# Kernel tuning notes

Measured on AMD Instinct MI355X. Metric: run time of the kernel, lower is better.

The kernel has to match this reference:

```python
import jax, jax.numpy as jnp
import numpy as np

EPS = 1e-5

def _relu6(x):
    return jnp.clip(x, 0.0, 6.0)

def _bn(x, g, b, m, v):
    # inference-mode batchnorm folded into scale/shift
    inv = g / jnp.sqrt(v + EPS)
    return x * inv[None, :, None, None] + (b - m * inv)[None, :, None, None]

def _patch_pw(x, W):
    # per-patch 1x1 conv. x: [B,Ci,H,Wd], W: [B,Fh,Fw,Co,Ci]
    B, C, H, Wd = x.shape
    Fh, Fw = W.shape[1:3]
    ph, pw = H // Fh, Wd // Fw
    xb = x.reshape(B, C, Fh, ph, Fw, pw)
    yb = jnp.einsum('bfgoc,bcfpgq->bofpgq', W, xb)
    return yb.reshape(B, W.shape[3], H, Wd)

def _patch_dw3(x, K):
    # per-patch depthwise 3x3, reflect pad applied to the full map (halo from neighbors).
    # x: [B,C,H,Wd], K: [B,Fh,Fw,C,3,3]
    B, C, H, Wd = x.shape
    Fh, Fw = K.shape[1:3]
    ph, pw = H // Fh, Wd // Fw
    xp = jnp.pad(x, ((0, 0), (0, 0), (1, 1), (1, 1)), mode='reflect')
    acc = jnp.zeros((B, C, Fh, ph, Fw, pw), x.dtype)
    for dy in range(3):
        for dx in range(3):
            xs = xp[:, :, dy:dy + H, dx:dx + Wd].reshape(B, C, Fh, ph, Fw, pw)
            k = K[:, :, :, :, dy, dx].transpose(0, 3, 1, 2)  # [B,C,Fh,Fw]
            acc = acc + xs * k[:, :, :, None, :, None]
    return acc.reshape(B, C, H, Wd)

def setup_inputs() -> dict:
    key = jax.random.key(0)
    ks = jax.random.split(key, 16)
    B, Cin, H, Wd = 4, 64, 128, 128
    hidden, Cout, Fh, Fw = 384, 64, 16, 16
    n_params = hidden * Cin + hidden * 9 + Cout * hidden  # 52608
    return {
        'x': jax.random.normal(ks[0], (B, Cin, H, Wd), jnp.float32),
        'w': jax.random.normal(ks[1], (B, n_params, Fh, Fw), jnp.float32) * 0.05,
        'g1': jax.random.uniform(ks[2], (hidden,), jnp.float32),
        'b1': jax.random.normal(ks[3], (hidden,), jnp.float32),
        'm1': jax.random.normal(ks[4], (hidden,), jnp.float32),
        'v1': jax.random.uniform(ks[5], (hidden,), jnp.float32),
        'g2': jax.random.uniform(ks[6], (hidden,), jnp.float32),
        'b2': jax.random.normal(ks[7], (hidden,), jnp.float32),
        'm2': jax.random.normal(ks[8], (hidden,), jnp.float32),
        'v2': jax.random.uniform(ks[9], (hidden,), jnp.float32),
        'g3': jax.random.uniform(ks[10], (Cout,), jnp.float32),
        'b3': jax.random.normal(ks[11], (Cout,), jnp.float32),
        'm3': jax.random.normal(ks[12], (Cout,), jnp.float32),
        'v3': jax.random.uniform(ks[13], (Cout,), jnp.float32),
    }

def reference(x, w, g1, b1, m1, v1, g2, b2, m2, v2, g3, b3, m3, v3):
    B, Cin = x.shape[:2]
    Fh, Fw = w.shape[2:]
    hidden = g1.shape[0]
    Cout = g3.shape[0]
    n1 = hidden * Cin
    n2 = hidden * 9
    wg = w.transpose(0, 2, 3, 1)  # [B,Fh,Fw,P]
    W1 = wg[..., :n1].reshape(B, Fh, Fw, hidden, Cin)
    K2 = wg[..., n1:n1 + n2].reshape(B, Fh, Fw, hidden, 3, 3)
    W3 = wg[..., n1 + n2:].reshape(B, Fh, Fw, Cout, hidden)
    h = _relu6(_bn(_patch_pw(x, W1), g1, b1, m1, v1))
    h = _relu6(_bn(_patch_dw3(h, K2), g2, b2, m2, v2))
    h = _bn(_patch_pw(h, W3), g3, b3, m3, v3)
    return x + h  # use_res_connect: stride==1 and in_nc==out_nc
```

## Files before the change

### kernel.cpp

```cpp
#include <hip/hip_runtime.h>

#define EPSV 1e-5f

constexpr int CIN = 64, NH = 128, NW = 128, HID = 384, COUT = 64;
constexpr int N1 = HID * CIN;
constexpr int N2 = HID * 9;
constexpr int NP = N1 + N2 + COUT * HID;

using bf16x8 = __attribute__((ext_vector_type(8))) short;
using f32x4  = __attribute__((ext_vector_type(4))) float;

__device__ __forceinline__ unsigned short f2bf(float f) {
  unsigned int u = __float_as_uint(f);
  u = (u + 0x7fffu + ((u >> 16) & 1u)) >> 16;
  return (unsigned short)u;
}
__device__ __forceinline__ unsigned int pack2(float a, float b) {
  return (unsigned int)f2bf(a) | ((unsigned int)f2bf(b) << 16);
}
__device__ __forceinline__ float ulo(unsigned int u) { return __uint_as_float(u << 16); }
__device__ __forceinline__ float uhi(unsigned int u) { return __uint_as_float(u & 0xffff0000u); }
__device__ __forceinline__ float clamp6(float v) { return fminf(fmaxf(v, 0.f), 6.f); }

__global__ __launch_bounds__(256) void k0_transpose(
    const float* __restrict__ x, unsigned short* __restrict__ xT) {
  __shared__ unsigned short xls[64][66];
  const int t = threadIdx.x;
  const int xh = blockIdx.x, y = blockIdx.y, b = blockIdx.z;
#pragma unroll
  for (int it = 0; it < 4; ++it) {
    int i = it * 256 + t;
    int xq = i & 15, c = i >> 4;
    float4 v = *reinterpret_cast<const float4*>(
        &x[((size_t)(b * CIN + c) * NH + y) * NW + xh * 64 + xq * 4]);
    *(unsigned int*)&xls[c][xq * 4]     = pack2(v.x, v.y);
    *(unsigned int*)&xls[c][xq * 4 + 2] = pack2(v.z, v.w);
  }
  __syncthreads();
#pragma unroll
  for (int it = 0; it < 4; ++it) {
    int i = it * 256 + t;
    int cq = i & 15, px = i >> 4;
    ushort4 o;
    o.x = xls[cq * 4 + 0][px];
    o.y = xls[cq * 4 + 1][px];
    o.z = xls[cq * 4 + 2][px];
    o.w = xls[cq * 4 + 3][px];
    *reinterpret_cast<ushort4*>(
        &xT[((size_t)(b * NH + y) * NW + xh * 64 + px) * 64 + cq * 4]) = o;
  }
}

__global__ __launch_bounds__(256) void k1_pw1(
    const float* __restrict__ w, const unsigned short* __restrict__ xT,
    const float* __restrict__ g1, const float* __restrict__ b1,
    const float* __restrict__ m1, const float* __restrict__ v1,
    unsigned short* __restrict__ h1T) {
  __shared__ unsigned short Wpk[2048 * 8];

  const unsigned int id = blockIdx.x;
  const int fbq = id & 7;
  const unsigned int rest = id >> 3;
  const int hgrp = rest % 24, q = rest / 24;
  const int fb = q * 8 + fbq;
  const int f = fb & 15, b = fb >> 4;
  const int h0 = hgrp * 16;

  const int t = threadIdx.x;
  const int lane = t & 63, wv = t >> 6;
  const int quad = lane >> 4, nn = lane & 15;
  const int pxi = wv * 16 + nn;

#pragma unroll
  for (int it = 0; it < 8; ++it) {
    int i = it * 256 + t;
    int gq = i & 3, cp = (i >> 2) & 31, hid = i >> 7;
    const float* wp =
        &w[((size_t)b * NP + (h0 + hid) * CIN + cp * 2) * 256 + f * 16 + gq * 4];
    float4 A  = *reinterpret_cast<const float4*>(wp);
    float4 Bv = *reinterpret_cast<const float4*>(wp + 256);
    int kc = cp >> 4, qd = (cp >> 2) & 3, j = (cp & 3) * 2;
    int hs = hid ^ (2 * qd) ^ gq;
    const float* Af = (const float*)&A;
    const float* Bf = (const float*)&Bv;
#pragma unroll
    for (int k = 0; k < 4; ++k) {
      int g = gq * 4 + k;
      *(unsigned int*)&Wpk[(((g * 2 + kc) * 4 + qd) * 16 + hs) * 8 + j] =
          pack2(Af[k], Bf[k]);
    }
  }

  float iv1[4], sh1[4];
#pragma unroll
  for (int jj = 0; jj < 4; ++jj) {
    int hid = h0 + quad * 4 + jj;
    float iv = g1[hid] * rsqrtf(v1[hid] + EPSV);
    iv1[jj] = iv;
    sh1[jj] = b1[hid] - m1[hid] * iv;
  }
  __syncthreads();

  const int y = f * 8 + (pxi >> 3);
  const size_t rowbase = ((size_t)b * NH + y) * NW;

  for (int g = 0; g < 16; ++g) {
    const int xc = g * 8 + (pxi & 7);
    const unsigned short* xp = &xT[(rowbase + xc) * 64];
    f32x4 acc = {0.f, 0.f, 0.f, 0.f};
    const int hs = nn ^ (2 * quad) ^ (g >> 2);
#pragma unroll
    for (int kc = 0; kc < 2; ++kc) {
      bf16x8 af = *reinterpret_cast<const bf16x8*>(
          &Wpk[(((g * 2 + kc) * 4 + quad) * 16 + hs) * 8]);
      bf16x8 bfr = *reinterpret_cast<const bf16x8*>(&xp[kc * 32 + quad * 8]);
      acc = __builtin_amdgcn_mfma_f32_16x16x32_bf16(af, bfr, acc, 0, 0, 0);
    }
    ushort4 o;
    o.x = f2bf(clamp6(acc[0] * iv1[0] + sh1[0]));
    o.y = f2bf(clamp6(acc[1] * iv1[1] + sh1[1]));
    o.z = f2bf(clamp6(acc[2] * iv1[2] + sh1[2]));
    o.w = f2bf(clamp6(acc[3] * iv1[3] + sh1[3]));
    *reinterpret_cast<ushort4*>(&h1T[(rowbase + xc) * HID + h0 + quad * 4]) = o;
  }
}

__global__ __launch_bounds__(256) void k2_fused(
    const float* __restrict__ x, const float* __restrict__ w,
    const float* __restrict__ g2, const float* __restrict__ b2v,
    const float* __restrict__ m2, const float* __restrict__ v2,
    const float* __restrict__ g3, const float* __restrict__ b3v,
    const float* __restrict__ m3, const float* __restrict__ v3,
    const unsigned short* __restrict__ h1T, float* __restrict__ out) {
  __shared__ unsigned short tile[10][34][40];
  __shared__ unsigned short h2s[256][40];
  __shared__ unsigned short W3p[512 * 8];
  __shared__ unsigned short k2w[4][9][40];
  __shared__ float iv2s[HID], sh2s[HID];

  const unsigned int id = blockIdx.x;
  const int fbq = id & 7;
  const unsigned int rest = id >> 3;
  const int gang = rest & 7, q = rest >> 3;
  const int fb = q * 8 + fbq;
  const int f = fb & 15, b = fb >> 4;
  const int gq = gang >> 1, ch = gang & 1;
  const int c0 = gq * 32;

  const int t = threadIdx.x;
  const int lane = t & 63, wv = t >> 6;
  const int quad = lane >> 4, nn = lane & 15;

  for (int i = t; i < HID; i += 256) {
    float iv = g2[i] * rsqrtf(v2[i] + EPSV);
    iv2s[i] = iv;
    sh2s[i] = b2v[i] - m2[i] * iv;
  }

  float iv3[2][4], sh3[2][4];
#pragma unroll
  for (int cot = 0; cot < 2; ++cot)
#pragma unroll
    for (int jj = 0; jj < 4; ++jj) {
      int co = ch * 32 + cot * 16 + quad * 4 + jj;
      float iv = g3[co] * rsqrtf(v3[co] + EPSV);
      iv3[cot][jj] = iv;
      sh3[cot][jj] = b3v[co] - m3[co] * iv;
    }

  f32x4 acc[2][4];
#pragma unroll
  for (int cot = 0; cot < 2; ++cot)
#pragma unroll
    for (int nt = 0; nt < 4; ++nt) acc[cot][nt] = (f32x4){0.f, 0.f, 0.f, 0.f};

  const int glt = t >> 6, rt = (t >> 3) & 7, ct = t & 7;

  for (int hc = 0; hc < 12; ++hc) {
    const int hb = hc * 32;
    __syncthreads();

#pragma unroll
    for (int it = 0; it < 6; ++it) {
      int idx = it * 256 + t;
      if (idx < 1360) {
        int qh = idx & 3, pxid = idx >> 2;
        int r = pxid / 34, col = pxid - r * 34;
        int yy = f * 8 - 1 + r;
        yy = (yy < 0) ? -yy : ((yy > 127) ? 254 - yy : yy);
        int xc = c0 - 1 + col;
        xc = (xc < 0) ? 1 : ((xc > 127) ? 126 : xc);
        uint4 v = *reinterpret_cast<const uint4*>(
            &h1T[(((size_t)b * NH + yy) * NW + xc) * HID + hb + qh * 8]);
        *reinterpret_cast<uint4*>(&tile[r][col][qh * 8]) = v;
      }
    }
    for (int i = t; i < 288; i += 256) {
      int hh = i / 9, tap = i - hh * 9;
      const float4 wv4 = *reinterpret_cast<const float4*>(
          &w[((size_t)b * NP + N1 + (hb + hh) * 9 + tap) * 256 + f * 16 +
             gq * 4]);
      k2w[0][tap][hh] = f2bf(wv4.x);
      k2w[1][tap][hh] = f2bf(wv4.y);
      k2w[2][tap][hh] = f2bf(wv4.z);
      k2w[3][tap][hh] = f2bf(wv4.w);
    }
#pragma unroll
    for (int it = 0; it < 2; ++it) {
      int i = it * 256 + t;
      int hhp = i & 15, co = i >> 4;
      const float* wp = &w[((size_t)b * NP + N1 + N2 + (ch * 32 + co) * HID +
                            hb + hhp * 2) * 256 + f * 16 + gq * 4];
      float4 A  = *reinterpret_cast<const float4*>(wp);
      float4 Bv = *reinterpret_cast<const float4*>(wp + 256);
      int qd = (hhp * 2) >> 3, j = (hhp * 2) & 7, cot = co >> 4;
      int cb = co & 15;
      const float* Af = (const float*)&A;
      const float* Bf = (const float*)&Bv;
#pragma unroll
      for (int k = 0; k < 4; ++k) {
        int cop = cb ^ (2 * qd) ^ k;
        *(unsigned int*)&W3p[(((k * 2 + cot) * 4 + qd) * 16 + cop) * 8 + j] =
            pack2(Af[k], Bf[k]);
      }
    }
    __syncthreads();

#pragma unroll
    for (int hg = 0; hg < 4; ++hg) {
      float d[8] = {0.f, 0.f, 0.f, 0.f, 0.f, 0.f, 0.f, 0.f};
#pragma unroll
      for (int dy = 0; dy < 3; ++dy)
#pragma unroll
        for (int dx = 0; dx < 3; ++dx) {
          const uint4 tv = *reinterpret_cast<const uint4*>(
              &tile[rt + dy][glt * 8 + ct + dx][hg * 8]);
          const uint4 kv =
              *reinterpret_cast<const uint4*>(&k2w[glt][dy * 3 + dx][hg * 8]);
          d[0] += ulo(tv.x) * ulo(kv.x); d[1] += uhi(tv.x) * uhi(kv.x);
          d[2] += ulo(tv.y) * ulo(kv.y); d[3] += uhi(tv.y) * uhi(kv.y);
          d[4] += ulo(tv.z) * ulo(kv.z); d[5] += uhi(tv.z) * uhi(kv.z);
          d[6] += ulo(tv.w) * ulo(kv.w); d[7] += uhi(tv.w) * uhi(kv.w);
        }
      uint4 o4;
      unsigned int op[4];
#pragma unroll
      for (int j2 = 0; j2 < 4; ++j2) {
        int ha = hb + hg * 8 + j2 * 2;
        float oa = clamp6(d[j2 * 2] * iv2s[ha] + sh2s[ha]);
        float ob = clamp6(d[j2 * 2 + 1] * iv2s[ha + 1] + sh2s[ha + 1]);
        op[j2] = (unsigned int)f2bf(oa) | ((unsigned int)f2bf(ob) << 16);
      }
      o4.x = op[0]; o4.y = op[1]; o4.z = op[2]; o4.w = op[3];
      *reinterpret_cast<uint4*>(&h2s[t][hg * 8]) = o4;
    }
    __syncthreads();

    {
      const int gl = wv;
      const int cop = nn ^ (2 * quad) ^ gl;
      bf16x8 a0 = *reinterpret_cast<const bf16x8*>(
          &W3p[(((gl * 2 + 0) * 4 + quad) * 16 + cop) * 8]);
      bf16x8 a1 = *reinterpret_cast<const bf16x8*>(
          &W3p[(((gl * 2 + 1) * 4 + quad) * 16 + cop) * 8]);
#pragma unroll
      for (int nt = 0; nt < 4; ++nt) {
        bf16x8 bfr = *reinterpret_cast<const bf16x8*>(
            &h2s[gl * 64 + nt * 16 + nn][quad * 8]);
        acc[0][nt] = __builtin_amdgcn_mfma_f32_16x16x32_bf16(a0, bfr, acc[0][nt], 0, 0, 0);
        acc[1][nt] = __builtin_amdgcn_mfma_f32_16x16x32_bf16(a1, bfr, acc[1][nt], 0, 0, 0);
      }
    }
  }

#pragma unroll
  for (int cot = 0; cot < 2; ++cot)
#pragma unroll
    for (int nt = 0; nt < 4; ++nt) {
      int pxl = nt * 16 + nn;
      int y = f * 8 + (pxl >> 3);
      int xc = c0 + wv * 8 + (pxl & 7);
#pragma unroll
      for (int jj = 0; jj < 4; ++jj) {
        int co = ch * 32 + cot * 16 + quad * 4 + jj;
        size_t adr = ((size_t)(b * COUT + co) * NH + y) * NW + xc;
        out[adr] = acc[cot][nt][jj] * iv3[cot][jj] + sh3[cot][jj] + x[adr];
      }
    }
}

extern "C" void kernel_launch(void* const* d_in, const int* in_sizes, int n_in,
                              void* d_out, int out_size, void* d_ws,
                              size_t ws_size, hipStream_t stream) {
  (void)in_sizes; (void)n_in; (void)out_size; (void)ws_size;
  const float* x  = (const float*)d_in[0];
  const float* w  = (const float*)d_in[1];
  const float* g1 = (const float*)d_in[2];
  const float* b1 = (const float*)d_in[3];
  const float* m1 = (const float*)d_in[4];
  const float* v1 = (const float*)d_in[5];
  const float* g2 = (const float*)d_in[6];
  const float* b2 = (const float*)d_in[7];
  const float* m2 = (const float*)d_in[8];
  const float* v2 = (const float*)d_in[9];
  const float* g3 = (const float*)d_in[10];
  const float* b3 = (const float*)d_in[11];
  const float* m3 = (const float*)d_in[12];
  const float* v3 = (const float*)d_in[13];
  float* out = (float*)d_out;
  unsigned short* h1T = (unsigned short*)d_ws;
  unsigned short* xT = (unsigned short*)d_out;

  k0_transpose<<<dim3(2, 128, 4), 256, 0, stream>>>(x, xT);
  k1_pw1<<<dim3(1536), 256, 0, stream>>>(w, xT, g1, b1, m1, v1, h1T);
  k2_fused<<<dim3(512), 256, 0, stream>>>(x, w, g2, b2, m2, v2, g3, b3, m3, v3,
                                          h1T, out);
}
```

Baseline: 460.3 us.

## Register-prefetch next hidden chunk's tile and weights to overlap global loads with compute

Moves the global loads for the next 32-channel hidden chunk (h1 halo tile, depthwise kernels, W3 slice) into registers issued right after the LDS-store barrier, so they overlap with the depthwise and MFMA work of the current chunk. Address computations are hoisted out of the loop into precomputed pointers that advance each iteration. __syncthreads is replaced by an explicit lgkmcnt wait plus s_barrier, which does not wait on outstanding global loads. This costs many extra VGPRs for the prefetch buffers and pointers, which may reduce occupancy.

```diff
diff --git a/kernel.cpp b/kernel.cpp
--- a/kernel.cpp
+++ b/kernel.cpp
@@ -21,6 +21,12 @@
 __device__ __forceinline__ float ulo(unsigned int u) { return __uint_as_float(u << 16); }
 __device__ __forceinline__ float uhi(unsigned int u) { return __uint_as_float(u & 0xffff0000u); }
 __device__ __forceinline__ float clamp6(float v) { return fminf(fmaxf(v, 0.f), 6.f); }
+
+#define BAR_LDS()                                             \
+  do {                                                        \
+    asm volatile("s_waitcnt lgkmcnt(0)" ::: "memory");        \
+    __builtin_amdgcn_s_barrier();                             \
+  } while (0)
 
 __global__ __launch_bounds__(256) void k0_transpose(
     const float* __restrict__ x, unsigned short* __restrict__ xT) {
@@ -176,55 +182,97 @@
 
   const int glt = t >> 6, rt = (t >> 3) & 7, ct = t & 7;
 
+  const unsigned short* tsrc[6];
+  unsigned short* tdst[6];
+  bool tac[6];
+#pragma unroll
+  for (int it = 0; it < 6; ++it) {
+    int idx = it * 256 + t;
+    tac[it] = (idx < 1360);
+    int idc = tac[it] ? idx : 0;
+    int qh = idc & 3, pxid = idc >> 2;
+    int r = pxid / 34, col = pxid - r * 34;
+    int yy = f * 8 - 1 + r;
+    yy = (yy < 0) ? -yy : ((yy > 127) ? 254 - yy : yy);
+    int xc = c0 - 1 + col;
+    xc = (xc < 0) ? 1 : ((xc > 127) ? 126 : xc);
+    tsrc[it] = &h1T[(((size_t)b * NH + yy) * NW + xc) * HID + qh * 8];
+    tdst[it] = &tile[r][col][qh * 8];
+  }
+  const int hh1 = t / 9, tap1 = t - hh1 * 9;
+  const float* ksrc1 = &w[((size_t)b * NP + N1 + t) * 256 + f * 16 + gq * 4];
+  const bool kac2 = (t < 32);
+  const int i2k = 256 + t;
+  const int hh2 = i2k / 9, tap2 = i2k - hh2 * 9;
+  const float* ksrc2 = &w[((size_t)b * NP + N1 + i2k) * 256 + f * 16 + gq * 4];
+  const float* wsrc[2];
+  unsigned int* wdst[2][4];
+#pragma unroll
+  for (int it = 0; it < 2; ++it) {
+    int i = it * 256 + t;
+    int hhp = i & 15, co = i >> 4;
+    wsrc[it] = &w[((size_t)b * NP + N1 + N2 + (ch * 32 + co) * HID + hhp * 2) *
+                      256 + f * 16 + gq * 4];
+    int qd = (hhp * 2) >> 3, j = (hhp * 2) & 7, cot = co >> 4, cb = co & 15;
+#pragma unroll
+    for (int k = 0; k < 4; ++k) {
+      int cop = cb ^ (2 * qd) ^ k;
+      wdst[it][k] =
+          (unsigned int*)&W3p[(((k * 2 + cot) * 4 + qd) * 16 + cop) * 8 + j];
+    }
+  }
+
+  uint4 trg[6];
+  float4 krg1, krg2;
+  float4 wAr[2], wBr[2];
+
+#define PREFETCH()                                                           \
+  do {                                                                       \
+    _Pragma("unroll") for (int pit = 0; pit < 6; ++pit) {                    \
+      if (tac[pit]) trg[pit] = *reinterpret_cast<const uint4*>(tsrc[pit]);   \
+      tsrc[pit] += 32;                                       \
+    }                                                                        \
+    krg1 = *reinterpret_cast<const float4*>(ksrc1);                          \
+    ksrc1 += 73728;                                            \
+    if (kac2) krg2 = *reinterpret_cast<const float4*>(ksrc2);                \
+    ksrc2 += 73728;                                                          \
+    _Pragma("unroll") for (int pit = 0; pit < 2; ++pit) {                    \
+      wAr[pit] = *reinterpret_cast<const float4*>(wsrc[pit]);                \
+      wBr[pit] = *reinterpret_cast<const float4*>(wsrc[pit] + 256);          \
+      wsrc[pit] += 8192;                                         \
+    }                                                                        \
+  } while (0)
+
+  PREFETCH();
+
   for (int hc = 0; hc < 12; ++hc) {
     const int hb = hc * 32;
-    __syncthreads();
-
-#pragma unroll
-    for (int it = 0; it < 6; ++it) {
-      int idx = it * 256 + t;
-      if (idx < 1360) {
-        int qh = idx & 3, pxid = idx >> 2;
-        int r = pxid / 34, col = pxid - r * 34;
-        int yy = f * 8 - 1 + r;
-        yy = (yy < 0) ? -yy : ((yy > 127) ? 254 - yy : yy);
-        int xc = c0 - 1 + col;
-        xc = (xc < 0) ? 1 : ((xc > 127) ? 126 : xc);
-        uint4 v = *reinterpret_cast<const uint4*>(
-            &h1T[(((size_t)b * NH + yy) * NW + xc) * HID + hb + qh * 8]);
-        *reinterpret_cast<uint4*>(&tile[r][col][qh * 8]) = v;
-      }
-    }
-    for (int i = t; i < 288; i += 256) {
-      int hh = i / 9, tap = i - hh * 9;
-      const float4 wv4 = *reinterpret_cast<const float4*>(
-          &w[((size_t)b * NP + N1 + (hb + hh) * 9 + tap) * 256 + f * 16 +
-             gq * 4]);
-      k2w[0][tap][hh] = f2bf(wv4.x);
-      k2w[1][tap][hh] = f2bf(wv4.y);
-      k2w[2][tap][hh] = f2bf(wv4.z);
-      k2w[3][tap][hh] = f2bf(wv4.w);
+    BAR_LDS();
+
+#pragma unroll
+    for (int it = 0; it < 6; ++it)
+      if (tac[it]) *reinterpret_cast<uint4*>(tdst[it]) = trg[it];
+    k2w[0][tap1][hh1] = f2bf(krg1.x);
+    k2w[1][tap1][hh1] = f2bf(krg1.y);
+    k2w[2][tap1][hh1] = f2bf(krg1.z);
+    k2w[3][tap1][hh1] = f2bf(krg1.w);
+    if (kac2) {
+      k2w[0][tap2][hh2] = f2bf(krg2.x);
+      k2w[1][tap2][hh2] = f2bf(krg2.y);
+      k2w[2][tap2][hh2] = f2bf(krg2.z);
+      k2w[3][tap2][hh2] = f2bf(krg2.w);
     }
 #pragma unroll
     for (int it = 0; it < 2; ++it) {
-      int i = it * 256 + t;
-      int hhp = i & 15, co = i >> 4;
-      const float* wp = &w[((size_t)b * NP + N1 + N2 + (ch * 32 + co) * HID +
-                            hb + hhp * 2) * 256 + f * 16 + gq * 4];
-      float4 A  = *reinterpret_cast<const float4*>(wp);
-      float4 Bv = *reinterpret_cast<const float4*>(wp + 256);
-      int qd = (hhp * 2) >> 3, j = (hhp * 2) & 7, cot = co >> 4;
-      int cb = co & 15;
-      const float* Af = (const float*)&A;
-      const float* Bf = (const float*)&Bv;
-#pragma unroll
-      for (int k = 0; k < 4; ++k) {
-        int cop = cb ^ (2 * qd) ^ k;
-        *(unsigned int*)&W3p[(((k * 2 + cot) * 4 + qd) * 16 + cop) * 8 + j] =
-            pack2(Af[k], Bf[k]);
-      }
-    }
-    __syncthreads();
+      const float* Af = (const float*)&wAr[it];
+      const float* Bf = (const float*)&wBr[it];
+#pragma unroll
+      for (int k = 0; k < 4; ++k) *wdst[it][k] = pack2(Af[k], Bf[k]);
+    }
+
+    BAR_LDS();
+
+    if (hc < 11) PREFETCH();
 
 #pragma unroll
     for (int hg = 0; hg < 4; ++hg) {
@@ -254,7 +302,8 @@
       o4.x = op[0]; o4.y = op[1]; o4.z = op[2]; o4.w = op[3];
       *reinterpret_cast<uint4*>(&h2s[t][hg * 8]) = o4;
     }
-    __syncthreads();
+
+    BAR_LDS();
 
     {
       const int gl = wv;
```

After: 492.0 us. 1.07x slower.

## Register-prefetch next chunk's h1 tile and weights to overlap global loads with compute

Applied to the files above, without the earlier changes.

The fused depthwise+pointwise kernel now issues global loads for the next hidden-channel chunk (h1 tile, depthwise taps, W3 weights) into registers right after the LDS stores. Those loads overlap with the depthwise and MFMA compute of the current chunk. Per-thread source and destination addresses are precomputed once and advanced by strides, and __syncthreads is replaced with a waitcnt on LDS only plus a raw barrier. Launch bounds request two blocks per SM, which adds register pressure from the prefetch registers and risks spills.

```diff
diff --git a/kernel.cpp b/kernel.cpp
--- a/kernel.cpp
+++ b/kernel.cpp
@@ -21,6 +21,12 @@
 __device__ __forceinline__ float ulo(unsigned int u) { return __uint_as_float(u << 16); }
 __device__ __forceinline__ float uhi(unsigned int u) { return __uint_as_float(u & 0xffff0000u); }
 __device__ __forceinline__ float clamp6(float v) { return fminf(fmaxf(v, 0.f), 6.f); }
+
+#define BAR_LDS()                                             \
+  do {                                                        \
+    asm volatile("s_waitcnt lgkmcnt(0)" ::: "memory");        \
+    __builtin_amdgcn_s_barrier();                             \
+  } while (0)
 
 __global__ __launch_bounds__(256) void k0_transpose(
     const float* __restrict__ x, unsigned short* __restrict__ xT) {
@@ -125,7 +131,7 @@
   }
 }
 
-__global__ __launch_bounds__(256) void k2_fused(
+__global__ __launch_bounds__(256, 2) void k2_fused(
     const float* __restrict__ x, const float* __restrict__ w,
     const float* __restrict__ g2, const float* __restrict__ b2v,
     const float* __restrict__ m2, const float* __restrict__ v2,
@@ -176,55 +182,121 @@
 
   const int glt = t >> 6, rt = (t >> 3) & 7, ct = t & 7;
 
+#define TGEOM(IDX, SRC, DST)                                          \
+  {                                                                   \
+    int qh = (IDX) & 3, pxid = (IDX) >> 2;                            \
+    int r = pxid / 34, col = pxid - r * 34;                           \
+    int yy = f * 8 - 1 + r;                                           \
+    yy = (yy < 0) ? -yy : ((yy > 127) ? 254 - yy : yy);               \
+    int xc = c0 - 1 + col;                                            \
+    xc = (xc < 0) ? 1 : ((xc > 127) ? 126 : xc);                      \
+    SRC = &h1T[(((size_t)b * NH + yy) * NW + xc) * HID + qh * 8];     \
+    DST = &tile[r][col][qh * 8];                                      \
+  }
+  const unsigned short *ts0, *ts1, *ts2, *ts3, *ts4, *ts5;
+  unsigned short *td0, *td1, *td2, *td3, *td4, *td5;
+  const bool tac5 = (t < 80);
+  TGEOM(t, ts0, td0);
+  TGEOM(256 + t, ts1, td1);
+  TGEOM(512 + t, ts2, td2);
+  TGEOM(768 + t, ts3, td3);
+  TGEOM(1024 + t, ts4, td4);
+  {
+    int idx5 = tac5 ? (1280 + t) : 1359;
+    TGEOM(idx5, ts5, td5);
+  }
+#undef TGEOM
+
+  const int hh1 = t / 9, tap1 = t - hh1 * 9;
+  const float* ksrc1 = &w[((size_t)b * NP + N1 + t) * 256 + f * 16 + gq * 4];
+  const bool kac2 = (t < 32);
+  const int i2k = 256 + t;
+  const int hh2 = i2k / 9, tap2 = i2k - hh2 * 9;
+  const float* ksrc2 = &w[((size_t)b * NP + N1 + i2k) * 256 + f * 16 + gq * 4];
+
+  const float *wsrc0, *wsrc1;
+  unsigned int *wd00, *wd01, *wd02, *wd03, *wd10, *wd11, *wd12, *wd13;
+#define W3GEOM(IT, SRC, D0, D1, D2, D3)                                   \
+  {                                                                      \
+    int i = (IT) * 256 + t;                                              \
+    int hhp = i & 15, co = i >> 4;                                       \
+    SRC = &w[((size_t)b * NP + N1 + N2 + (ch * 32 + co) * HID + hhp * 2) * \
+                 256 + f * 16 + gq * 4];                                 \
+    int qd = (hhp * 2) >> 3, j = (hhp * 2) & 7, cot = co >> 4,           \
+        cb = co & 15;                                                    \
+    D0 = (unsigned int*)&W3p[(((0 * 2 + cot) * 4 + qd) * 16 +            \
+                              (cb ^ (2 * qd) ^ 0)) * 8 + j];             \
+    D1 = (unsigned int*)&W3p[(((1 * 2 + cot) * 4 + qd) * 16 +            \
+                              (cb ^ (2 * qd) ^ 1)) * 8 + j];             \
+    D2 = (unsigned int*)&W3p[(((2 * 2 + cot) * 4 + qd) * 16 +            \
+                              (cb ^ (2 * qd) ^ 2)) * 8 + j];             \
+    D3 = (unsigned int*)&W3p[(((3 * 2 + cot) * 4 + qd) * 16 +            \
+                              (cb ^ (2 * qd) ^ 3)) * 8 + j];             \
+  }
+  W3GEOM(0, wsrc0, wd00, wd01, wd02, wd03);
+  W3GEOM(1, wsrc1, wd10, wd11, wd12, wd13);
+#undef W3GEOM
+
+  uint4 tr0, tr1, tr2, tr3, tr4, tr5;
+  float4 kr1, kr2;
+  float4 wA0, wB0, wA1, wB1;
+
+#define PREFETCH()                                                  \
+  do {                                                              \
+    tr0 = *reinterpret_cast<const uint4*>(ts0); ts0 += 32;          \
+    tr1 = *reinterpret_cast<const uint4*>(ts1); ts1 += 32;          \
+    tr2 = *reinterpret_cast<const uint4*>(ts2); ts2 += 32;          \
+    tr3 = *reinterpret_cast<const uint4*>(ts3); ts3 += 32;          \
+    tr4 = *reinterpret_cast<const uint4*>(ts4); ts4 += 32;          \
+    if (tac5) tr5 = *reinterpret_cast<const uint4*>(ts5);           \
+    ts5 += 32;                                                      \
+    kr1 = *reinterpret_cast<const float4*>(ksrc1); ksrc1 += 73728;  \
+    if (kac2) kr2 = *reinterpret_cast<const float4*>(ksrc2);        \
+    ksrc2 += 73728;                                                 \
+    wA0 = *reinterpret_cast<const float4*>(wsrc0);                  \
+    wB0 = *reinterpret_cast<const float4*>(wsrc0 + 256);            \
+    wsrc0 += 8192;                                                  \
+    wA1 = *reinterpret_cast<const float4*>(wsrc1);                  \
+    wB1 = *reinterpret_cast<const float4*>(wsrc1 + 256);            \
+    wsrc1 += 8192;                                                  \
+  } while (0)
+
+  tr5 = (uint4){0u, 0u, 0u, 0u};
+  kr2 = (float4){0.f, 0.f, 0.f, 0.f};
+  PREFETCH();
+
   for (int hc = 0; hc < 12; ++hc) {
     const int hb = hc * 32;
-    __syncthreads();
-
-#pragma unroll
-    for (int it = 0; it < 6; ++it) {
-      int idx = it * 256 + t;
-      if (idx < 1360) {
-        int qh = idx & 3, pxid = idx >> 2;
-        int r = pxid / 34, col = pxid - r * 34;
-        int yy = f * 8 - 1 + r;
-        yy = (yy < 0) ? -yy : ((yy > 127) ? 254 - yy : yy);
-        int xc = c0 - 1 + col;
-        xc = (xc < 0) ? 1 : ((xc > 127) ? 126 : xc);
-        uint4 v = *reinterpret_cast<const uint4*>(
-            &h1T[(((size_t)b * NH + yy) * NW + xc) * HID + hb + qh * 8]);
-        *reinterpret_cast<uint4*>(&tile[r][col][qh * 8]) = v;
-      }
-    }
-    for (int i = t; i < 288; i += 256) {
-      int hh = i / 9, tap = i - hh * 9;
-      const float4 wv4 = *reinterpret_cast<const float4*>(
-          &w[((size_t)b * NP + N1 + (hb + hh) * 9 + tap) * 256 + f * 16 +
-             gq * 4]);
-      k2w[0][tap][hh] = f2bf(wv4.x);
-      k2w[1][tap][hh] = f2bf(wv4.y);
-      k2w[2][tap][hh] = f2bf(wv4.z);
-      k2w[3][tap][hh] = f2bf(wv4.w);
-    }
-#pragma unroll
-    for (int it = 0; it < 2; ++it) {
-      int i = it * 256 + t;
-      int hhp = i & 15, co = i >> 4;
-      const float* wp = &w[((size_t)b * NP + N1 + N2 + (ch * 32 + co) * HID +
-                            hb + hhp * 2) * 256 + f * 16 + gq * 4];
-      float4 A  = *reinterpret_cast<const float4*>(wp);
-      float4 Bv = *reinterpret_cast<const float4*>(wp + 256);
-      int qd = (hhp * 2) >> 3, j = (hhp * 2) & 7, cot = co >> 4;
-      int cb = co & 15;
-      const float* Af = (const float*)&A;
-      const float* Bf = (const float*)&Bv;
-#pragma unroll
-      for (int k = 0; k < 4; ++k) {
-        int cop = cb ^ (2 * qd) ^ k;
-        *(unsigned int*)&W3p[(((k * 2 + cot) * 4 + qd) * 16 + cop) * 8 + j] =
-            pack2(Af[k], Bf[k]);
-      }
-    }
-    __syncthreads();
+    BAR_LDS();
+
+    *reinterpret_cast<uint4*>(td0) = tr0;
+    *reinterpret_cast<uint4*>(td1) = tr1;
+    *reinterpret_cast<uint4*>(td2) = tr2;
+    *reinterpret_cast<uint4*>(td3) = tr3;
+    *reinterpret_cast<uint4*>(td4) = tr4;
+    if (tac5) *reinterpret_cast<uint4*>(td5) = tr5;
+    k2w[0][tap1][hh1] = f2bf(kr1.x);
+    k2w[1][tap1][hh1] = f2bf(kr1.y);
+    k2w[2][tap1][hh1] = f2bf(kr1.z);
+    k2w[3][tap1][hh1] = f2bf(kr1.w);
+    if (kac2) {
+      k2w[0][tap2][hh2] = f2bf(kr2.x);
+      k2w[1][tap2][hh2] = f2bf(kr2.y);
+      k2w[2][tap2][hh2] = f2bf(kr2.z);
+      k2w[3][tap2][hh2] = f2bf(kr2.w);
+    }
+    *wd00 = pack2(wA0.x, wB0.x);
+    *wd01 = pack2(wA0.y, wB0.y);
+    *wd02 = pack2(wA0.z, wB0.z);
+    *wd03 = pack2(wA0.w, wB0.w);
+    *wd10 = pack2(wA1.x, wB1.x);
+    *wd11 = pack2(wA1.y, wB1.y);
+    *wd12 = pack2(wA1.z, wB1.z);
+    *wd13 = pack2(wA1.w, wB1.w);
+
+    BAR_LDS();
+
+    if (hc < 11) PREFETCH();
 
 #pragma unroll
     for (int hg = 0; hg < 4; ++hg) {
@@ -254,7 +326,8 @@
       o4.x = op[0]; o4.y = op[1]; o4.z = op[2]; o4.w = op[3];
       *reinterpret_cast<uint4*>(&h2s[t][hg * 8]) = o4;
     }
-    __syncthreads();
+
+    BAR_LDS();
 
     {
       const int gl = wv;
```

Measured after the change: 440.1 us. 4.4% less time.
